# Optimization experiments

Measured on AMD Instinct MI355X. Metric: run time of the kernel, lower is better.

The kernel has to match this reference:

```python
import math
import jax, jax.numpy as jnp
import numpy as np

BASE = 10000.0
SCALING_FACTOR = 1.0
ORIG_MAX_POS = 4096
BETA_FAST, BETA_SLOW = 32, 1
MSCALE = 0.707
MSCALE_ALL_DIM = 0.707


def _yarn_cos_sin(seq_len: int, dim: int):
    # DeepseekV3YarnRotaryEmbedding._set_cos_sin_cache, computed in numpy (constants)
    def corr_dim(num_rot):
        return dim * math.log(ORIG_MAX_POS / (num_rot * 2 * math.pi)) / (2 * math.log(BASE))
    low = max(math.floor(corr_dim(BETA_FAST)), 0)
    high = min(math.ceil(corr_dim(BETA_SLOW)), dim - 1)
    hi = high + 0.001 if low == high else high
    ramp = np.clip((np.arange(dim // 2, dtype=np.float32) - low) / (hi - low), 0.0, 1.0)
    inv_freq_mask = 1.0 - ramp
    freq_extra = 1.0 / BASE ** (np.arange(0, dim, 2, dtype=np.float32) / dim)
    freq_inter = freq_extra / SCALING_FACTOR
    inv_freq = freq_inter * (1.0 - inv_freq_mask) + freq_extra * inv_freq_mask
    t = np.arange(seq_len, dtype=np.float32)
    freqs = np.outer(t, inv_freq)
    def get_mscale(s, m):
        return 1.0 if s <= 1 else 0.1 * m * math.log(s) + 1.0
    _m = get_mscale(SCALING_FACTOR, MSCALE) / get_mscale(SCALING_FACTOR, MSCALE_ALL_DIM)
    emb = np.concatenate([freqs, freqs], axis=-1)  # [S, dim]
    return jnp.asarray(np.cos(emb) * _m), jnp.asarray(np.sin(emb) * _m)


def _rotate_half(x):
    x1, x2 = jnp.split(x, 2, axis=-1)
    return jnp.concatenate([-x2, x1], axis=-1)


def setup_inputs() -> dict:
    key = jax.random.key(0)
    ks = jax.random.split(key, 5)
    B, S, H, DN, DR, DV = 2, 2048, 16, 128, 64, 128
    return {
        "q_nope": jax.random.normal(ks[0], (B, S, H, DN), jnp.float32),
        "q_pe": jax.random.normal(ks[1], (B, S, H, DR), jnp.float32),
        "k_nope": jax.random.normal(ks[2], (B, S, H, DN), jnp.float32),
        "k_pe": jax.random.normal(ks[3], (B, S, 1, DR), jnp.float32),  # shared rope key head
        "v": jax.random.normal(ks[4], (B, S, H, DV), jnp.float32),
    }


def reference(q_nope, q_pe, k_nope, k_pe, v):
    B, S, H, DN = q_nope.shape
    DR = q_pe.shape[-1]
    sm_scale = (DN + DR) ** (-0.5)  # qk_head_dim**-0.5
    cos, sin = _yarn_cos_sin(S, DR)  # [S, DR]
    cos = cos[None, :, None, :]
    sin = sin[None, :, None, :]
    # decoupled RoPE on the rope slice (apply_rotary_pos_emb with position_ids=arange)
    qp = q_pe * cos + _rotate_half(q_pe) * sin              # [B,S,H,DR]
    kp = k_pe * cos + _rotate_half(k_pe) * sin              # [B,S,1,DR]
    kp = jnp.broadcast_to(kp, (B, S, H, DR))
    q = jnp.concatenate([q_nope, qp], axis=-1)              # [B,S,H,DN+DR]
    k = jnp.concatenate([k_nope, kp], axis=-1)
    # attention_ref: full fp32 logits, causal mask, lse*log2(e), softmax, PV
    logits = jnp.einsum('bmhd,bnhd->bhmn', q.astype(jnp.float32), k.astype(jnp.float32)) * sm_scale
    mask = jnp.arange(S)[:, None] >= jnp.arange(S)[None, :]  # qo_len == kv_len
    logits = jnp.where(mask[None, None], logits, -jnp.inf)
    lse = jnp.transpose(jax.scipy.special.logsumexp(logits, axis=-1), (0, 2, 1)) * math.log2(math.e)
    p = jax.nn.softmax(logits, axis=-1)
    o = jnp.einsum('bhmn,bnhd->bmhd', p, v.astype(jnp.float32))
    o = o.reshape(B * S, H, -1).astype(q_nope.dtype)        # [B*S, H, DV]
    return o, lse
```

## Files before the change

kernel.cpp:

```cpp
#include <hip/hip_runtime.h>
#include <hip/hip_bf16.h>
#include <math.h>

#define NB 2
#define SEQ 2048
#define NH 16
#define DNOPE 128
#define DROT 64
#define DVDIM 128
#define DQK 192
#define BM 64
#define BN 64

typedef __bf16 bf16x8_t __attribute__((ext_vector_type(8)));
typedef float f32x4_t __attribute__((ext_vector_type(4)));

#define LOG2_BASE_OVER_HALFDIM 0.41524101186092028f
#define KSL2 0.10412340175817158f

#define KBF_ELEMS   ((size_t)NB * NH * SEQ * DQK)
#define KPREP_BLOCKS 6144
#define VPREP_BLOCKS 1024

__global__ __launch_bounds__(256) void prep_kernel(
    const float* __restrict__ k_nope, const float* __restrict__ k_pe,
    const float* __restrict__ v, __bf16* __restrict__ Kbf,
    __bf16* __restrict__ Vtb) {
  __shared__ __bf16 T[64][130];
  const int bid = blockIdx.x;
  const int tid = threadIdx.x;
  if (bid < KPREP_BLOCKS) {
    int gid = bid * 256 + tid;
    size_t o8 = (size_t)gid * 8;
    int d0 = (int)(o8 % DQK);
    int rest = (int)(o8 / DQK);
    int s = rest & (SEQ - 1);
    int bh = rest >> 11;
    int h = bh & (NH - 1), b = bh >> 4;
    bf16x8_t o;
    if (d0 < DNOPE) {
      const float* p = k_nope + ((size_t)((b * SEQ + s) * NH + h)) * DNOPE + d0;
      float4 a = *(const float4*)p;
      float4 c = *(const float4*)(p + 4);
      o[0] = (__bf16)a.x; o[1] = (__bf16)a.y; o[2] = (__bf16)a.z; o[3] = (__bf16)a.w;
      o[4] = (__bf16)c.x; o[5] = (__bf16)c.y; o[6] = (__bf16)c.z; o[7] = (__bf16)c.w;
    } else {
      int dr0 = d0 - DNOPE;
      const float* p = k_pe + (size_t)(b * SEQ + s) * DROT;
#pragma unroll
      for (int j = 0; j < 8; ++j) {
        int dr = dr0 + j;
        int i = dr & 31;
        float invf = exp2f(-LOG2_BASE_OVER_HALFDIM * (float)i);
        float ang = (float)s * invf;
        float sn, cs; sincosf(ang, &sn, &cs);
        float x = p[dr];
        float oth = (dr < 32) ? -p[dr + 32] : p[dr - 32];
        o[j] = (__bf16)(x * cs + oth * sn);
      }
    }
    *(bf16x8_t*)&Kbf[o8] = o;
  } else {
    int vb = bid - KPREP_BLOCKS;
    const int s0 = (vb & 31) * 64, h = (vb >> 5) & (NH - 1), b = vb >> 9;
#pragma unroll
    for (int r = 0; r < 8; ++r) {
      int task = tid + r * 256;
      int srow = task >> 5, c4 = (task & 31) * 4;
      const float* p = v + ((size_t)((b * SEQ + s0 + srow) * NH + h)) * DVDIM + c4;
      float4 a = *(const float4*)p;
      T[srow][c4 + 0] = (__bf16)a.x; T[srow][c4 + 1] = (__bf16)a.y;
      T[srow][c4 + 2] = (__bf16)a.z; T[srow][c4 + 3] = (__bf16)a.w;
    }
    __syncthreads();
#pragma unroll
    for (int r = 0; r < 4; ++r) {
      int task = tid + r * 256;
      int dv = task >> 3, c8 = (task & 7) * 8;
      bf16x8_t o;
#pragma unroll
      for (int u = 0; u < 8; ++u) o[u] = T[c8 + u][dv];
      *(bf16x8_t*)&Vtb[((size_t)(b * NH + h) * DVDIM + dv) * SEQ + s0 + c8] = o;
    }
  }
}

__global__ __launch_bounds__(256, 2) void mla_fwd_kernel(
    const float* __restrict__ q_nope, const float* __restrict__ q_pe,
    const __bf16* __restrict__ Kbf, const __bf16* __restrict__ Vtb,
    float* __restrict__ out_o, float* __restrict__ out_lse) {
  __shared__ __bf16 Kl[BN * DQK];
  __shared__ __bf16 Vl[DVDIM * BN];
  __shared__ __bf16 Pl[4 * 16 * BN];
  __shared__ __bf16 Vx[16 * 72];

  const int bx = blockIdx.x, h = blockIdx.y, b = blockIdx.z;
  const int tid = threadIdx.x;
  const int w = tid >> 6, lane = tid & 63;
  const int col = lane & 15, quad = lane >> 4;
  const int swz = col & 7;
  const int e0 = quad ^ swz, e1 = (quad + 4) ^ swz;

  for (int i = tid; i < 16 * 72; i += 256)
    Vx[i] = (i < 64) ? (__bf16)1.0f : (__bf16)0.0f;

  const __bf16* Kslab = Kbf + (size_t)(b * NH + h) * SEQ * DQK;
  const __bf16* Vslab = Vtb + (size_t)(b * NH + h) * DVDIM * SEQ;

  int kofs[6];
#pragma unroll
  for (int r = 0; r < 6; ++r) {
    int L = r * 256 + tid;
    int n = L / 24, jj = L - n * 24;
    int jsrc = (jj & ~7) | ((jj & 7) ^ (n & 7));
    kofs[r] = n * DQK + jsrc * 8;
  }
  int vofs[4];
#pragma unroll
  for (int r = 0; r < 4; ++r) {
    int L = r * 256 + tid;
    int dv = L >> 3, jj = L & 7;
    vofs[r] = dv * SEQ + (jj ^ (dv & 7)) * 8;
  }

  __syncthreads();
  const bf16x8_t vxf0 = *(const bf16x8_t*)&Vx[col * 72 + quad * 8];
  const bf16x8_t vxf1 = *(const bf16x8_t*)&Vx[col * 72 + 32 + quad * 8];

  for (int half = 0; half < 2; ++half) {
    const int qt = half ? bx : (31 - bx);
    const int qb = qt * BM;
    const int mrow = qb + w * 16 + col;

    const float* qn = q_nope + (size_t)((b * SEQ + mrow) * NH + h) * DNOPE;
    const float* qp = q_pe   + (size_t)((b * SEQ + mrow) * NH + h) * DROT;
    bf16x8_t qfrag[6];
#pragma unroll
    for (int c = 0; c < 4; ++c) {
      const float* p = qn + c * 32 + quad * 8;
      float4 a = *(const float4*)p;
      float4 bq = *(const float4*)(p + 4);
      bf16x8_t f;
      f[0]=(__bf16)(a.x*KSL2);  f[1]=(__bf16)(a.y*KSL2);
      f[2]=(__bf16)(a.z*KSL2);  f[3]=(__bf16)(a.w*KSL2);
      f[4]=(__bf16)(bq.x*KSL2); f[5]=(__bf16)(bq.y*KSL2);
      f[6]=(__bf16)(bq.z*KSL2); f[7]=(__bf16)(bq.w*KSL2);
      qfrag[c] = f;
    }
    {
      const float* plo = qp + quad * 8;
      const float* phi = qp + 32 + quad * 8;
      float4 lo0 = *(const float4*)plo;
      float4 lo1 = *(const float4*)(plo + 4);
      float4 hi0 = *(const float4*)phi;
      float4 hi1 = *(const float4*)(phi + 4);
      float xl[8] = {lo0.x,lo0.y,lo0.z,lo0.w,lo1.x,lo1.y,lo1.z,lo1.w};
      float xh[8] = {hi0.x,hi0.y,hi0.z,hi0.w,hi1.x,hi1.y,hi1.z,hi1.w};
      bf16x8_t f4v, f5v;
#pragma unroll
      for (int j = 0; j < 8; ++j) {
        int i = quad * 8 + j;
        float invf = exp2f(-LOG2_BASE_OVER_HALFDIM * (float)i);
        float ang = (float)mrow * invf;
        float sn, cs; sincosf(ang, &sn, &cs);
        f4v[j] = (__bf16)((xl[j] * cs - xh[j] * sn) * KSL2);
        f5v[j] = (__bf16)((xh[j] * cs + xl[j] * sn) * KSL2);
      }
      qfrag[4] = f4v; qfrag[5] = f5v;
    }

    f32x4_t oacc[8];
#pragma unroll
    for (int i = 0; i < 8; ++i) oacc[i] = (f32x4_t){0.f, 0.f, 0.f, 0.f};
    f32x4_t lacc = (f32x4_t){0.f, 0.f, 0.f, 0.f};
    float m_run[4] = {-INFINITY, -INFINITY, -INFINITY, -INFINITY};

    bf16x8_t Kreg[6], Vreg[4];
#pragma unroll
    for (int r = 0; r < 6; ++r) Kreg[r] = *(const bf16x8_t*)(Kslab + kofs[r]);
#pragma unroll
    for (int r = 0; r < 4; ++r) Vreg[r] = *(const bf16x8_t*)(Vslab + vofs[r]);

    for (int it = 0; it <= qt; ++it) {
      __syncthreads();
#pragma unroll
      for (int r = 0; r < 6; ++r) *(bf16x8_t*)&Kl[(r * 256 + tid) * 8] = Kreg[r];
#pragma unroll
      for (int r = 0; r < 4; ++r) *(bf16x8_t*)&Vl[(r * 256 + tid) * 8] = Vreg[r];
      __syncthreads();
      if (it < qt) {
        const __bf16* Ksrc = Kslab + (size_t)(it + 1) * BN * DQK;
        const __bf16* Vsrc = Vslab + (it + 1) * BN;
#pragma unroll
        for (int r = 0; r < 6; ++r) Kreg[r] = *(const bf16x8_t*)(Ksrc + kofs[r]);
#pragma unroll
        for (int r = 0; r < 4; ++r) Vreg[r] = *(const bf16x8_t*)(Vsrc + vofs[r]);
      }

      f32x4_t sacc[4];
#pragma unroll
      for (int t = 0; t < 4; ++t) sacc[t] = (f32x4_t){0.f, 0.f, 0.f, 0.f};
#pragma unroll
      for (int t = 0; t < 4; ++t) {
        const __bf16* kr = &Kl[(t * 16 + col) * 24 * 8];
        sacc[t] = __builtin_amdgcn_mfma_f32_16x16x32_bf16(qfrag[0], *(const bf16x8_t*)&kr[e0 * 8], sacc[t], 0, 0, 0);
        sacc[t] = __builtin_amdgcn_mfma_f32_16x16x32_bf16(qfrag[1], *(const bf16x8_t*)&kr[e1 * 8], sacc[t], 0, 0, 0);
        sacc[t] = __builtin_amdgcn_mfma_f32_16x16x32_bf16(qfrag[2], *(const bf16x8_t*)&kr[64 + e0 * 8], sacc[t], 0, 0, 0);
        sacc[t] = __builtin_amdgcn_mfma_f32_16x16x32_bf16(qfrag[3], *(const bf16x8_t*)&kr[64 + e1 * 8], sacc[t], 0, 0, 0);
        sacc[t] = __builtin_amdgcn_mfma_f32_16x16x32_bf16(qfrag[4], *(const bf16x8_t*)&kr[128 + e0 * 8], sacc[t], 0, 0, 0);
        sacc[t] = __builtin_amdgcn_mfma_f32_16x16x32_bf16(qfrag[5], *(const bf16x8_t*)&kr[128 + e1 * 8], sacc[t], 0, 0, 0);
      }

      const bool diag = (it == qt);
      float pv[4][4];
      float alpha[4];
#pragma unroll
      for (int r = 0; r < 4; ++r) {
        float mx = -INFINITY;
#pragma unroll
        for (int t = 0; t < 4; ++t) {
          float sv = sacc[t][r];
          if (diag) {
            int nn = (qt << 6) + t * 16 + col;
            int mm = qb + w * 16 + quad * 4 + r;
            if (nn > mm) sv = -INFINITY;
          }
          pv[t][r] = sv;
          mx = fmaxf(mx, sv);
        }
        mx = fmaxf(mx, __shfl_xor(mx, 1, 64));
        mx = fmaxf(mx, __shfl_xor(mx, 2, 64));
        mx = fmaxf(mx, __shfl_xor(mx, 4, 64));
        mx = fmaxf(mx, __shfl_xor(mx, 8, 64));
        float mnew = fmaxf(m_run[r], mx);
        alpha[r] = exp2f(m_run[r] - mnew);
        m_run[r] = mnew;
#pragma unroll
        for (int t = 0; t < 4; ++t) pv[t][r] = exp2f(pv[t][r] - mnew);
      }
#pragma unroll
      for (int d = 0; d < 8; ++d) {
        f32x4_t o = oacc[d];
        o[0] *= alpha[0]; o[1] *= alpha[1]; o[2] *= alpha[2]; o[3] *= alpha[3];
        oacc[d] = o;
      }
      lacc[0] *= alpha[0]; lacc[1] *= alpha[1];
      lacc[2] *= alpha[2]; lacc[3] *= alpha[3];

      __bf16* Pw = &Pl[w * 16 * BN];
#pragma unroll
      for (int t = 0; t < 4; ++t)
#pragma unroll
        for (int r = 0; r < 4; ++r) {
          int row = quad * 4 + r;
          int j = t * 2 + (col >> 3);
          Pw[(row * 8 + (j ^ (row & 7))) * 8 + (col & 7)] = (__bf16)pv[t][r];
        }
      bf16x8_t pf0 = *(const bf16x8_t*)&Pw[(col * 8 + e0) * 8];
      bf16x8_t pf1 = *(const bf16x8_t*)&Pw[(col * 8 + e1) * 8];

#pragma unroll
      for (int d = 0; d < 8; ++d) {
        const __bf16* vr = &Vl[(d * 16 + col) * 64];
        bf16x8_t vf0 = *(const bf16x8_t*)&vr[e0 * 8];
        bf16x8_t vf1 = *(const bf16x8_t*)&vr[e1 * 8];
        oacc[d] = __builtin_amdgcn_mfma_f32_16x16x32_bf16(pf0, vf0, oacc[d], 0, 0, 0);
        oacc[d] = __builtin_amdgcn_mfma_f32_16x16x32_bf16(pf1, vf1, oacc[d], 0, 0, 0);
      }
      lacc = __builtin_amdgcn_mfma_f32_16x16x32_bf16(pf0, vxf0, lacc, 0, 0, 0);
      lacc = __builtin_amdgcn_mfma_f32_16x16x32_bf16(pf1, vxf1, lacc, 0, 0, 0);
    }

    float lr[4];
#pragma unroll
    for (int r = 0; r < 4; ++r) lr[r] = __shfl(lacc[r], lane & 48, 64);
    float inv_l[4];
#pragma unroll
    for (int r = 0; r < 4; ++r) inv_l[r] = 1.0f / lr[r];
#pragma unroll
    for (int d = 0; d < 8; ++d) {
#pragma unroll
      for (int r = 0; r < 4; ++r) {
        int mm = qb + w * 16 + quad * 4 + r;
        out_o[(size_t)((b * SEQ + mm) * NH + h) * DVDIM + d * 16 + col] = oacc[d][r] * inv_l[r];
      }
    }
    if (col < 4) {
      int r = col;
      int mm = qb + w * 16 + quad * 4 + r;
      out_lse[(size_t)(b * SEQ + mm) * NH + h] = m_run[r] + log2f(lr[r]);
    }
  }
}

extern "C" void kernel_launch(void* const* d_in, const int* in_sizes, int n_in,
                              void* d_out, int out_size, void* d_ws, size_t ws_size,
                              hipStream_t stream) {
  const float* q_nope = (const float*)d_in[0];
  const float* q_pe   = (const float*)d_in[1];
  const float* k_nope = (const float*)d_in[2];
  const float* k_pe   = (const float*)d_in[3];
  const float* v      = (const float*)d_in[4];
  float* out_o   = (float*)d_out;
  float* out_lse = out_o + (size_t)NB * SEQ * NH * DVDIM;

  __bf16* Kbf = (__bf16*)d_ws;
  __bf16* Vtb = Kbf + KBF_ELEMS;

  prep_kernel<<<dim3(KPREP_BLOCKS + VPREP_BLOCKS), dim3(256), 0, stream>>>(
      k_nope, k_pe, v, Kbf, Vtb);
  mla_fwd_kernel<<<dim3(16, NH, NB), dim3(256), 0, stream>>>(
      q_nope, q_pe, Kbf, Vtb, out_o, out_lse);
}
```

Baseline: 264.6 us.

## Launch one block per Q tile with XCD-aware heavy-first ordering

Replaces the paired-tile scheme, where each block processed a heavy and a light causal Q tile, with a flat 1024-block grid holding one Q tile per block. Block IDs are mapped so that the heaviest tiles come first and each (batch, head) stays on one XCD, which should improve L2 reuse of K/V. The launch bound is raised to 3 blocks per CU, and the shared-memory ones-vector used for the row-sum MFMA is replaced by a register constant. Load balance now depends on the hardware scheduler picking up tail work, and the tighter register budget may cause spills.

```diff
diff --git a/kernel.cpp b/kernel.cpp
--- a/kernel.cpp
+++ b/kernel.cpp
@@ -85,24 +85,32 @@
   }
 }
 
-__global__ __launch_bounds__(256, 2) void mla_fwd_kernel(
+__global__ __launch_bounds__(256, 3) void mla_fwd_kernel(
     const float* __restrict__ q_nope, const float* __restrict__ q_pe,
     const __bf16* __restrict__ Kbf, const __bf16* __restrict__ Vtb,
     float* __restrict__ out_o, float* __restrict__ out_lse) {
   __shared__ __bf16 Kl[BN * DQK];
   __shared__ __bf16 Vl[DVDIM * BN];
   __shared__ __bf16 Pl[4 * 16 * BN];
-  __shared__ __bf16 Vx[16 * 72];
-
-  const int bx = blockIdx.x, h = blockIdx.y, b = blockIdx.z;
+
+  const int bid = blockIdx.x;
+  const int xcd = bid & 7;
+  const int j   = bid >> 3;
+  const int sl  = j & 3;
+  const int qt  = 31 - (j >> 2);
+  const int g   = sl * 8 + xcd;
+  const int h   = g & (NH - 1), b = g >> 4;
+
   const int tid = threadIdx.x;
   const int w = tid >> 6, lane = tid & 63;
   const int col = lane & 15, quad = lane >> 4;
   const int swz = col & 7;
   const int e0 = quad ^ swz, e1 = (quad + 4) ^ swz;
 
-  for (int i = tid; i < 16 * 72; i += 256)
-    Vx[i] = (i < 64) ? (__bf16)1.0f : (__bf16)0.0f;
+  const __bf16 onev = (col == 0) ? (__bf16)1.0f : (__bf16)0.0f;
+  bf16x8_t vxf;
+#pragma unroll
+  for (int u = 0; u < 8; ++u) vxf[u] = onev;
 
   const __bf16* Kslab = Kbf + (size_t)(b * NH + h) * SEQ * DQK;
   const __bf16* Vslab = Vtb + (size_t)(b * NH + h) * DVDIM * SEQ;
@@ -123,173 +131,166 @@
     vofs[r] = dv * SEQ + (jj ^ (dv & 7)) * 8;
   }
 
-  __syncthreads();
-  const bf16x8_t vxf0 = *(const bf16x8_t*)&Vx[col * 72 + quad * 8];
-  const bf16x8_t vxf1 = *(const bf16x8_t*)&Vx[col * 72 + 32 + quad * 8];
-
-  for (int half = 0; half < 2; ++half) {
-    const int qt = half ? bx : (31 - bx);
-    const int qb = qt * BM;
-    const int mrow = qb + w * 16 + col;
-
-    const float* qn = q_nope + (size_t)((b * SEQ + mrow) * NH + h) * DNOPE;
-    const float* qp = q_pe   + (size_t)((b * SEQ + mrow) * NH + h) * DROT;
-    bf16x8_t qfrag[6];
-#pragma unroll
-    for (int c = 0; c < 4; ++c) {
-      const float* p = qn + c * 32 + quad * 8;
-      float4 a = *(const float4*)p;
-      float4 bq = *(const float4*)(p + 4);
-      bf16x8_t f;
-      f[0]=(__bf16)(a.x*KSL2);  f[1]=(__bf16)(a.y*KSL2);
-      f[2]=(__bf16)(a.z*KSL2);  f[3]=(__bf16)(a.w*KSL2);
-      f[4]=(__bf16)(bq.x*KSL2); f[5]=(__bf16)(bq.y*KSL2);
-      f[6]=(__bf16)(bq.z*KSL2); f[7]=(__bf16)(bq.w*KSL2);
-      qfrag[c] = f;
-    }
-    {
-      const float* plo = qp + quad * 8;
-      const float* phi = qp + 32 + quad * 8;
-      float4 lo0 = *(const float4*)plo;
-      float4 lo1 = *(const float4*)(plo + 4);
-      float4 hi0 = *(const float4*)phi;
-      float4 hi1 = *(const float4*)(phi + 4);
-      float xl[8] = {lo0.x,lo0.y,lo0.z,lo0.w,lo1.x,lo1.y,lo1.z,lo1.w};
-      float xh[8] = {hi0.x,hi0.y,hi0.z,hi0.w,hi1.x,hi1.y,hi1.z,hi1.w};
-      bf16x8_t f4v, f5v;
-#pragma unroll
-      for (int j = 0; j < 8; ++j) {
-        int i = quad * 8 + j;
-        float invf = exp2f(-LOG2_BASE_OVER_HALFDIM * (float)i);
-        float ang = (float)mrow * invf;
-        float sn, cs; sincosf(ang, &sn, &cs);
-        f4v[j] = (__bf16)((xl[j] * cs - xh[j] * sn) * KSL2);
-        f5v[j] = (__bf16)((xh[j] * cs + xl[j] * sn) * KSL2);
+  const int qb = qt * BM;
+  const int mrow = qb + w * 16 + col;
+
+  const float* qn = q_nope + (size_t)((b * SEQ + mrow) * NH + h) * DNOPE;
+  const float* qp = q_pe   + (size_t)((b * SEQ + mrow) * NH + h) * DROT;
+  bf16x8_t qfrag[6];
+#pragma unroll
+  for (int c = 0; c < 4; ++c) {
+    const float* p = qn + c * 32 + quad * 8;
+    float4 a = *(const float4*)p;
+    float4 bq = *(const float4*)(p + 4);
+    bf16x8_t f;
+    f[0]=(__bf16)(a.x*KSL2);  f[1]=(__bf16)(a.y*KSL2);
+    f[2]=(__bf16)(a.z*KSL2);  f[3]=(__bf16)(a.w*KSL2);
+    f[4]=(__bf16)(bq.x*KSL2); f[5]=(__bf16)(bq.y*KSL2);
+    f[6]=(__bf16)(bq.z*KSL2); f[7]=(__bf16)(bq.w*KSL2);
+    qfrag[c] = f;
+  }
+  {
+    const float* plo = qp + quad * 8;
+    const float* phi = qp + 32 + quad * 8;
+    float4 lo0 = *(const float4*)plo;
+    float4 lo1 = *(const float4*)(plo + 4);
+    float4 hi0 = *(const float4*)phi;
+    float4 hi1 = *(const float4*)(phi + 4);
+    float xl[8] = {lo0.x,lo0.y,lo0.z,lo0.w,lo1.x,lo1.y,lo1.z,lo1.w};
+    float xh[8] = {hi0.x,hi0.y,hi0.z,hi0.w,hi1.x,hi1.y,hi1.z,hi1.w};
+    bf16x8_t f4v, f5v;
+#pragma unroll
+    for (int jr = 0; jr < 8; ++jr) {
+      int i = quad * 8 + jr;
+      float invf = exp2f(-LOG2_BASE_OVER_HALFDIM * (float)i);
+      float ang = (float)mrow * invf;
+      float sn, cs; sincosf(ang, &sn, &cs);
+      f4v[jr] = (__bf16)((xl[jr] * cs - xh[jr] * sn) * KSL2);
+      f5v[jr] = (__bf16)((xh[jr] * cs + xl[jr] * sn) * KSL2);
+    }
+    qfrag[4] = f4v; qfrag[5] = f5v;
+  }
+
+  f32x4_t oacc[8];
+#pragma unroll
+  for (int i = 0; i < 8; ++i) oacc[i] = (f32x4_t){0.f, 0.f, 0.f, 0.f};
+  f32x4_t lacc = (f32x4_t){0.f, 0.f, 0.f, 0.f};
+  float m_run[4] = {-INFINITY, -INFINITY, -INFINITY, -INFINITY};
+
+  bf16x8_t Kreg[6], Vreg[4];
+#pragma unroll
+  for (int r = 0; r < 6; ++r) Kreg[r] = *(const bf16x8_t*)(Kslab + kofs[r]);
+#pragma unroll
+  for (int r = 0; r < 4; ++r) Vreg[r] = *(const bf16x8_t*)(Vslab + vofs[r]);
+
+  for (int it = 0; it <= qt; ++it) {
+    __syncthreads();
+#pragma unroll
+    for (int r = 0; r < 6; ++r) *(bf16x8_t*)&Kl[(r * 256 + tid) * 8] = Kreg[r];
+#pragma unroll
+    for (int r = 0; r < 4; ++r) *(bf16x8_t*)&Vl[(r * 256 + tid) * 8] = Vreg[r];
+    __syncthreads();
+    if (it < qt) {
+      const __bf16* Ksrc = Kslab + (size_t)(it + 1) * BN * DQK;
+      const __bf16* Vsrc = Vslab + (it + 1) * BN;
+#pragma unroll
+      for (int r = 0; r < 6; ++r) Kreg[r] = *(const bf16x8_t*)(Ksrc + kofs[r]);
+#pragma unroll
+      for (int r = 0; r < 4; ++r) Vreg[r] = *(const bf16x8_t*)(Vsrc + vofs[r]);
+    }
+
+    f32x4_t sacc[4];
+#pragma unroll
+    for (int t = 0; t < 4; ++t) sacc[t] = (f32x4_t){0.f, 0.f, 0.f, 0.f};
+#pragma unroll
+    for (int t = 0; t < 4; ++t) {
+      const __bf16* kr = &Kl[(t * 16 + col) * 24 * 8];
+      sacc[t] = __builtin_amdgcn_mfma_f32_16x16x32_bf16(qfrag[0], *(const bf16x8_t*)&kr[e0 * 8], sacc[t], 0, 0, 0);
+      sacc[t] = __builtin_amdgcn_mfma_f32_16x16x32_bf16(qfrag[1], *(const bf16x8_t*)&kr[e1 * 8], sacc[t], 0, 0, 0);
+      sacc[t] = __builtin_amdgcn_mfma_f32_16x16x32_bf16(qfrag[2], *(const bf16x8_t*)&kr[64 + e0 * 8], sacc[t], 0, 0, 0);
+      sacc[t] = __builtin_amdgcn_mfma_f32_16x16x32_bf16(qfrag[3], *(const bf16x8_t*)&kr[64 + e1 * 8], sacc[t], 0, 0, 0);
+      sacc[t] = __builtin_amdgcn_mfma_f32_16x16x32_bf16(qfrag[4], *(const bf16x8_t*)&kr[128 + e0 * 8], sacc[t], 0, 0, 0);
+      sacc[t] = __builtin_amdgcn_mfma_f32_16x16x32_bf16(qfrag[5], *(const bf16x8_t*)&kr[128 + e1 * 8], sacc[t], 0, 0, 0);
+    }
+
+    const bool diag = (it == qt);
+    float pv[4][4];
+    float alpha[4];
+#pragma unroll
+    for (int r = 0; r < 4; ++r) {
+      float mx = -INFINITY;
+#pragma unroll
+      for (int t = 0; t < 4; ++t) {
+        float sv = sacc[t][r];
+        if (diag) {
+          int nn = (qt << 6) + t * 16 + col;
+          int mm = qb + w * 16 + quad * 4 + r;
+          if (nn > mm) sv = -INFINITY;
+        }
+        pv[t][r] = sv;
+        mx = fmaxf(mx, sv);
       }
-      qfrag[4] = f4v; qfrag[5] = f5v;
-    }
-
-    f32x4_t oacc[8];
-#pragma unroll
-    for (int i = 0; i < 8; ++i) oacc[i] = (f32x4_t){0.f, 0.f, 0.f, 0.f};
-    f32x4_t lacc = (f32x4_t){0.f, 0.f, 0.f, 0.f};
-    float m_run[4] = {-INFINITY, -INFINITY, -INFINITY, -INFINITY};
-
-    bf16x8_t Kreg[6], Vreg[4];
-#pragma unroll
-    for (int r = 0; r < 6; ++r) Kreg[r] = *(const bf16x8_t*)(Kslab + kofs[r]);
-#pragma unroll
-    for (int r = 0; r < 4; ++r) Vreg[r] = *(const bf16x8_t*)(Vslab + vofs[r]);
-
-    for (int it = 0; it <= qt; ++it) {
-      __syncthreads();
-#pragma unroll
-      for (int r = 0; r < 6; ++r) *(bf16x8_t*)&Kl[(r * 256 + tid) * 8] = Kreg[r];
-#pragma unroll
-      for (int r = 0; r < 4; ++r) *(bf16x8_t*)&Vl[(r * 256 + tid) * 8] = Vreg[r];
-      __syncthreads();
-      if (it < qt) {
-        const __bf16* Ksrc = Kslab + (size_t)(it + 1) * BN * DQK;
-        const __bf16* Vsrc = Vslab + (it + 1) * BN;
-#pragma unroll
-        for (int r = 0; r < 6; ++r) Kreg[r] = *(const bf16x8_t*)(Ksrc + kofs[r]);
-#pragma unroll
-        for (int r = 0; r < 4; ++r) Vreg[r] = *(const bf16x8_t*)(Vsrc + vofs[r]);
+      mx = fmaxf(mx, __shfl_xor(mx, 1, 64));
+      mx = fmaxf(mx, __shfl_xor(mx, 2, 64));
+      mx = fmaxf(mx, __shfl_xor(mx, 4, 64));
+      mx = fmaxf(mx, __shfl_xor(mx, 8, 64));
+      float mnew = fmaxf(m_run[r], mx);
+      alpha[r] = exp2f(m_run[r] - mnew);
+      m_run[r] = mnew;
+#pragma unroll
+      for (int t = 0; t < 4; ++t) pv[t][r] = exp2f(pv[t][r] - mnew);
+    }
+#pragma unroll
+    for (int d = 0; d < 8; ++d) {
+      f32x4_t o = oacc[d];
+      o[0] *= alpha[0]; o[1] *= alpha[1]; o[2] *= alpha[2]; o[3] *= alpha[3];
+      oacc[d] = o;
+    }
+    lacc[0] *= alpha[0]; lacc[1] *= alpha[1];
+    lacc[2] *= alpha[2]; lacc[3] *= alpha[3];
+
+    __bf16* Pw = &Pl[w * 16 * BN];
+#pragma unroll
+    for (int t = 0; t < 4; ++t)
+#pragma unroll
+      for (int r = 0; r < 4; ++r) {
+        int row = quad * 4 + r;
+        int jj = t * 2 + (col >> 3);
+        Pw[(row * 8 + (jj ^ (row & 7))) * 8 + (col & 7)] = (__bf16)pv[t][r];
       }
-
-      f32x4_t sacc[4];
-#pragma unroll
-      for (int t = 0; t < 4; ++t) sacc[t] = (f32x4_t){0.f, 0.f, 0.f, 0.f};
-#pragma unroll
-      for (int t = 0; t < 4; ++t) {
-        const __bf16* kr = &Kl[(t * 16 + col) * 24 * 8];
-        sacc[t] = __builtin_amdgcn_mfma_f32_16x16x32_bf16(qfrag[0], *(const bf16x8_t*)&kr[e0 * 8], sacc[t], 0, 0, 0);
-        sacc[t] = __builtin_amdgcn_mfma_f32_16x16x32_bf16(qfrag[1], *(const bf16x8_t*)&kr[e1 * 8], sacc[t], 0, 0, 0);
-        sacc[t] = __builtin_amdgcn_mfma_f32_16x16x32_bf16(qfrag[2], *(const bf16x8_t*)&kr[64 + e0 * 8], sacc[t], 0, 0, 0);
-        sacc[t] = __builtin_amdgcn_mfma_f32_16x16x32_bf16(qfrag[3], *(const bf16x8_t*)&kr[64 + e1 * 8], sacc[t], 0, 0, 0);
-        sacc[t] = __builtin_amdgcn_mfma_f32_16x16x32_bf16(qfrag[4], *(const bf16x8_t*)&kr[128 + e0 * 8], sacc[t], 0, 0, 0);
-        sacc[t] = __builtin_amdgcn_mfma_f32_16x16x32_bf16(qfrag[5], *(const bf16x8_t*)&kr[128 + e1 * 8], sacc[t], 0, 0, 0);
-      }
-
-      const bool diag = (it == qt);
-      float pv[4][4];
-      float alpha[4];
-#pragma unroll
-      for (int r = 0; r < 4; ++r) {
-        float mx = -INFINITY;
-#pragma unroll
-        for (int t = 0; t < 4; ++t) {
-          float sv = sacc[t][r];
-          if (diag) {
-            int nn = (qt << 6) + t * 16 + col;
-            int mm = qb + w * 16 + quad * 4 + r;
-            if (nn > mm) sv = -INFINITY;
-          }
-          pv[t][r] = sv;
-          mx = fmaxf(mx, sv);
-        }
-        mx = fmaxf(mx, __shfl_xor(mx, 1, 64));
-        mx = fmaxf(mx, __shfl_xor(mx, 2, 64));
-        mx = fmaxf(mx, __shfl_xor(mx, 4, 64));
-        mx = fmaxf(mx, __shfl_xor(mx, 8, 64));
-        float mnew = fmaxf(m_run[r], mx);
-        alpha[r] = exp2f(m_run[r] - mnew);
-        m_run[r] = mnew;
-#pragma unroll
-        for (int t = 0; t < 4; ++t) pv[t][r] = exp2f(pv[t][r] - mnew);
-      }
-#pragma unroll
-      for (int d = 0; d < 8; ++d) {
-        f32x4_t o = oacc[d];
-        o[0] *= alpha[0]; o[1] *= alpha[1]; o[2] *= alpha[2]; o[3] *= alpha[3];
-        oacc[d] = o;
-      }
-      lacc[0] *= alpha[0]; lacc[1] *= alpha[1];
-      lacc[2] *= alpha[2]; lacc[3] *= alpha[3];
-
-      __bf16* Pw = &Pl[w * 16 * BN];
-#pragma unroll
-      for (int t = 0; t < 4; ++t)
-#pragma unroll
-        for (int r = 0; r < 4; ++r) {
-          int row = quad * 4 + r;
-          int j = t * 2 + (col >> 3);
-          Pw[(row * 8 + (j ^ (row & 7))) * 8 + (col & 7)] = (__bf16)pv[t][r];
-        }
-      bf16x8_t pf0 = *(const bf16x8_t*)&Pw[(col * 8 + e0) * 8];
-      bf16x8_t pf1 = *(const bf16x8_t*)&Pw[(col * 8 + e1) * 8];
-
-#pragma unroll
-      for (int d = 0; d < 8; ++d) {
-        const __bf16* vr = &Vl[(d * 16 + col) * 64];
-        bf16x8_t vf0 = *(const bf16x8_t*)&vr[e0 * 8];
-        bf16x8_t vf1 = *(const bf16x8_t*)&vr[e1 * 8];
-        oacc[d] = __builtin_amdgcn_mfma_f32_16x16x32_bf16(pf0, vf0, oacc[d], 0, 0, 0);
-        oacc[d] = __builtin_amdgcn_mfma_f32_16x16x32_bf16(pf1, vf1, oacc[d], 0, 0, 0);
-      }
-      lacc = __builtin_amdgcn_mfma_f32_16x16x32_bf16(pf0, vxf0, lacc, 0, 0, 0);
-      lacc = __builtin_amdgcn_mfma_f32_16x16x32_bf16(pf1, vxf1, lacc, 0, 0, 0);
-    }
-
-    float lr[4];
-#pragma unroll
-    for (int r = 0; r < 4; ++r) lr[r] = __shfl(lacc[r], lane & 48, 64);
-    float inv_l[4];
-#pragma unroll
-    for (int r = 0; r < 4; ++r) inv_l[r] = 1.0f / lr[r];
+    bf16x8_t pf0 = *(const bf16x8_t*)&Pw[(col * 8 + e0) * 8];
+    bf16x8_t pf1 = *(const bf16x8_t*)&Pw[(col * 8 + e1) * 8];
+
 #pragma unroll
     for (int d = 0; d < 8; ++d) {
-#pragma unroll
-      for (int r = 0; r < 4; ++r) {
-        int mm = qb + w * 16 + quad * 4 + r;
-        out_o[(size_t)((b * SEQ + mm) * NH + h) * DVDIM + d * 16 + col] = oacc[d][r] * inv_l[r];
-      }
-    }
-    if (col < 4) {
-      int r = col;
+      const __bf16* vr = &Vl[(d * 16 + col) * 64];
+      bf16x8_t vf0 = *(const bf16x8_t*)&vr[e0 * 8];
+      bf16x8_t vf1 = *(const bf16x8_t*)&vr[e1 * 8];
+      oacc[d] = __builtin_amdgcn_mfma_f32_16x16x32_bf16(pf0, vf0, oacc[d], 0, 0, 0);
+      oacc[d] = __builtin_amdgcn_mfma_f32_16x16x32_bf16(pf1, vf1, oacc[d], 0, 0, 0);
+    }
+    lacc = __builtin_amdgcn_mfma_f32_16x16x32_bf16(pf0, vxf, lacc, 0, 0, 0);
+    lacc = __builtin_amdgcn_mfma_f32_16x16x32_bf16(pf1, vxf, lacc, 0, 0, 0);
+  }
+
+  float lr[4];
+#pragma unroll
+  for (int r = 0; r < 4; ++r) lr[r] = __shfl(lacc[r], lane & 48, 64);
+  float inv_l[4];
+#pragma unroll
+  for (int r = 0; r < 4; ++r) inv_l[r] = 1.0f / lr[r];
+#pragma unroll
+  for (int d = 0; d < 8; ++d) {
+#pragma unroll
+    for (int r = 0; r < 4; ++r) {
       int mm = qb + w * 16 + quad * 4 + r;
-      out_lse[(size_t)(b * SEQ + mm) * NH + h] = m_run[r] + log2f(lr[r]);
-    }
+      out_o[(size_t)((b * SEQ + mm) * NH + h) * DVDIM + d * 16 + col] = oacc[d][r] * inv_l[r];
+    }
+  }
+  if (col < 4) {
+    int r = col;
+    int mm = qb + w * 16 + quad * 4 + r;
+    out_lse[(size_t)(b * SEQ + mm) * NH + h] = m_run[r] + log2f(lr[r]);
   }
 }
 
@@ -309,6 +310,6 @@
 
   prep_kernel<<<dim3(KPREP_BLOCKS + VPREP_BLOCKS), dim3(256), 0, stream>>>(
       k_nope, k_pe, v, Kbf, Vtb);
-  mla_fwd_kernel<<<dim3(16, NH, NB), dim3(256), 0, stream>>>(
+  mla_fwd_kernel<<<dim3(1024), dim3(256), 0, stream>>>(
       q_nope, q_pe, Kbf, Vtb, out_o, out_lse);
 }
```

After: 287.9 us. +8.8%, slower.
